# Optimization experiments

Measured on AMD Instinct MI355X. Metric: run time of the kernel, lower is better.

## Reference

```python
import jax, jax.numpy as jnp
import numpy as np

N = 768
SINGLE_DIM = 384
PAIR_DIM = 128
D = 16      # proj_dim per head
H = 12      # n_heads
P = 4       # n_query_points
PV = 8      # n_point_values


def _random_rotations(key, n):
    a = jax.random.normal(key, (n, 3, 3), dtype=jnp.float32)
    q, r = jnp.linalg.qr(a)
    d = jnp.sign(jnp.diagonal(r, axis1=-2, axis2=-1))
    q = q * d[:, None, :]
    det = jnp.linalg.det(q)
    return q * jnp.where(det < 0, -1.0, 1.0)[:, None, None]


def setup_inputs() -> dict:
    key = jax.random.key(0)
    ks = jax.random.split(key, 12)
    s = 0.02
    return {
        "single_rep": jax.random.normal(ks[0], (N, SINGLE_DIM), dtype=jnp.float32),
        "pair_rep": jax.random.normal(ks[1], (N, N, PAIR_DIM), dtype=jnp.float32),
        "rotations": _random_rotations(ks[2], N),
        "translations": jax.random.normal(ks[3], (N, 3), dtype=jnp.float32),
        "Wqkv": s * jax.random.normal(ks[4], (SINGLE_DIM, 3 * H * D), dtype=jnp.float32),
        "Wb": s * jax.random.normal(ks[5], (PAIR_DIM, H), dtype=jnp.float32),
        "Wqk_pts": s * jax.random.normal(ks[6], (SINGLE_DIM, 2 * H * P * 3), dtype=jnp.float32),
        "Wv_pts": s * jax.random.normal(ks[7], (SINGLE_DIM, H * PV * 3), dtype=jnp.float32),
        "gamma": 0.1 * jax.random.normal(ks[8], (H,), dtype=jnp.float32),
        "Wout": s * jax.random.normal(ks[9], (H * (PAIR_DIM + D + PV * 3 + PV), SINGLE_DIM), dtype=jnp.float32),
        "bout": jnp.zeros((SINGLE_DIM,), dtype=jnp.float32),
    }


def _apply_frames(rot, trans, pts):
    # pts: [N, P, H, 3] -> R @ pt + t per residue (dim 0)
    return jnp.einsum('nba,npha->nphb', rot, pts) + trans[:, None, None, :]


def _apply_frames_inv(rot, trans, pts):
    # R^T (pt - t)
    return jnp.einsum('nab,npha->nphb', rot, pts - trans[:, None, None, :])


def reference(single_rep, pair_rep, rotations, translations,
              Wqkv, Wb, Wqk_pts, Wv_pts, gamma, Wout, bout):
    n = single_rep.shape[0]
    sqrt_inv_dim = 1.0 / np.sqrt(D).astype(np.float32)
    w_C = np.sqrt(2.0 / (9.0 * P)).astype(np.float32)
    w_L = np.sqrt(1.0 / 3.0).astype(np.float32)

    qkv = single_rep @ Wqkv                       # [N, 3*H*D]
    q, k, v = jnp.split(qkv, 3, axis=-1)
    q = q.reshape(n, D, H)
    k = k.reshape(n, D, H)
    v = v.reshape(n, D, H)

    b = pair_rep @ Wb                             # [N, N, H]

    qk_pts = single_rep @ Wqk_pts
    q_pts, k_pts = jnp.split(qk_pts, 2, axis=-1)
    q_pts = jnp.moveaxis(q_pts.reshape(n, P, 3, H), -1, -2)   # [N, P, H, 3]
    k_pts = jnp.moveaxis(k_pts.reshape(n, P, 3, H), -1, -2)
    v_pts = jnp.moveaxis((single_rep @ Wv_pts).reshape(n, PV, 3, H), -1, -2)  # [N, PV, H, 3]

    qg = _apply_frames(rotations, translations, q_pts)  # [N, P, H, 3]
    kg = _apply_frames(rotations, translations, k_pts)

    # sum_{p,t} ||qg_i - kg_j||^2 via expansion (avoids [N,N,P,H,3])
    q_sq = jnp.sum(qg * qg, axis=(1, 3))                # [N, H]
    k_sq = jnp.sum(kg * kg, axis=(1, 3))                # [N, H]
    cross = jnp.einsum('ipht,jpht->ijh', qg, kg)        # [N, N, H]
    dist_logits = q_sq[:, None, :] + k_sq[None, :, :] - 2.0 * cross

    dp_logits = sqrt_inv_dim * jnp.einsum('idh,jdh->ijh', q, k) + b
    scale = gamma * (w_C / 2.0)                          # [H]
    a = jax.nn.softmax(w_L * (dp_logits - scale * dist_logits), axis=1)  # [N, N, H]

    out_pair = jnp.einsum('ijh,ijz->izh', a, pair_rep)   # [N, pair_dim, H]
    out_value = jnp.einsum('ijh,jdh->idh', a, v)          # [N, D, H]

    vg = _apply_frames(rotations, translations, v_pts)    # [N, PV, H, 3]
    op = jnp.einsum('ijh,jpht->ipht', a, vg)              # [N, PV, H, 3]
    out_points = _apply_frames_inv(rotations, translations, op)
    out_points_norm = jnp.linalg.norm(out_points, axis=-1)  # [N, PV, H]

    out = jnp.concatenate([
        out_pair.reshape(n, -1),
        out_value.reshape(n, -1),
        out_points.reshape(n, -1),
        out_points_norm.reshape(n, -1),
    ], axis=1)
    return out @ Wout + bout
```

## Files before the change

kernel.cpp:

```cpp
#include <hip/hip_runtime.h>
#include <math.h>

#define NN 768
#define SD 384
#define HH 12

#define W_L 0.57735026918962576f
#define W_C 0.23570226039551584f

__device__ __forceinline__ float dot32(const float* q, const float* k) {
  float s = 0.f;
  #pragma unroll
  for (int m = 0; m < 8; ++m) {
    float4 a = *(const float4*)(q + m*4);
    float4 b = *(const float4*)(k + m*4);
    s += a.x*b.x + a.y*b.y + a.z*b.z + a.w*b.w;
  }
  return s;
}

__global__ __launch_bounds__(256) void k1a_gemm(
    const float* __restrict__ single, const float* __restrict__ Wqkv,
    const float* __restrict__ Wqk, const float* __restrict__ Wvp,
    float* __restrict__ raw)
{
  __shared__ float Al[64][17];
  __shared__ float Bl[16][68];
  const int tid = threadIdx.x;
  const int bm = blockIdx.x / 18, bn = blockIdx.x % 18;
  const int tr = tid >> 4, tc = tid & 15;

  const int bcol = bn*64 + (tid & 15)*4;
  const float* Wsrc; int wstride;
  if (bcol < 576)      { Wsrc = Wqkv + bcol;        wstride = 576; }
  else if (bcol < 864) { Wsrc = Wqk  + (bcol-576);  wstride = 288; }
  else                 { Wsrc = Wvp  + (bcol-864);  wstride = 288; }
  const int brow = tid >> 4;
  const int ar = tid >> 2, ac = (tid & 3)*4;

  float4 acc0 = {0,0,0,0}, acc1 = {0,0,0,0}, acc2 = {0,0,0,0}, acc3 = {0,0,0,0};

  for (int kc = 0; kc < 24; ++kc) {
    __syncthreads();
    *(float4*)&Al[ar][ac] = *(const float4*)(single + (size_t)(bm*64+ar)*SD + kc*16 + ac);
    *(float4*)&Bl[brow][(tid&15)*4] = *(const float4*)(Wsrc + (size_t)(kc*16+brow)*wstride);
    __syncthreads();
    #pragma unroll
    for (int kk = 0; kk < 16; ++kk) {
      float a0 = Al[tr*4+0][kk], a1 = Al[tr*4+1][kk], a2 = Al[tr*4+2][kk], a3 = Al[tr*4+3][kk];
      float4 bv = *(float4*)&Bl[kk][tc*4];
      acc0.x += a0*bv.x; acc0.y += a0*bv.y; acc0.z += a0*bv.z; acc0.w += a0*bv.w;
      acc1.x += a1*bv.x; acc1.y += a1*bv.y; acc1.z += a1*bv.z; acc1.w += a1*bv.w;
      acc2.x += a2*bv.x; acc2.y += a2*bv.y; acc2.z += a2*bv.z; acc2.w += a2*bv.w;
      acc3.x += a3*bv.x; acc3.y += a3*bv.y; acc3.z += a3*bv.z; acc3.w += a3*bv.w;
    }
  }
  float* o = raw + (size_t)(bm*64 + tr*4)*1152 + bn*64 + tc*4;
  *(float4*)(o)            = acc0;
  *(float4*)(o + 1152)     = acc1;
  *(float4*)(o + 2*1152)   = acc2;
  *(float4*)(o + 3*1152)   = acc3;
}

__global__ __launch_bounds__(256) void k1b_pack(
    const float* __restrict__ raw_g, const float* __restrict__ rot,
    const float* __restrict__ trans, const float* __restrict__ gamma,
    float* __restrict__ Qt, float* __restrict__ Kt, float* __restrict__ vv)
{
  __shared__ float raw[4][1152];
  __shared__ float gbuf[4][16][HH][3];
  const int tid = threadIdx.x;
  const int i0 = blockIdx.x * 4;

  for (int s = tid; s < 4*288; s += 256) {
    int r = s / 288, q = s % 288;
    *(float4*)(&raw[r][q*4]) = *(const float4*)(raw_g + (size_t)(i0+r)*1152 + q*4);
  }
  __syncthreads();

  for (int s = tid; s < 4*576; s += 256) {
    int r = s / 576, cc = s % 576;
    int d = (cc % 192) / HH, h = cc % HH;
    int i = i0 + r;
    float val = raw[r][cc];
    if (cc < 192)       Qt[(size_t)i*384 + h*32 + d] = 0.25f*W_L*val;
    else if (cc < 384)  Kt[(size_t)i*384 + h*32 + d] = val;
    else                vv[(size_t)i*480 + h*40 + d] = val;
  }
  for (int s = tid; s < 768; s += 256) {
    int r = s / 192, rem = s % 192;
    int slot = rem / HH, h = rem % HH;
    int i = i0 + r;
    int base;
    if (slot < 4) base = 576 + slot*36;
    else if (slot < 8) base = 720 + (slot-4)*36;
    else base = 864 + (slot-8)*36;
    float x0 = raw[r][base + 0*12 + h];
    float x1 = raw[r][base + 1*12 + h];
    float x2 = raw[r][base + 2*12 + h];
    const float* R = rot + (size_t)i*9;
    const float* T = trans + (size_t)i*3;
    float g0 = R[0]*x0 + R[1]*x1 + R[2]*x2 + T[0];
    float g1 = R[3]*x0 + R[4]*x1 + R[5]*x2 + T[1];
    float g2 = R[6]*x0 + R[7]*x1 + R[8]*x2 + T[2];
    gbuf[r][slot][h][0]=g0; gbuf[r][slot][h][1]=g1; gbuf[r][slot][h][2]=g2;
    if (slot < 4) {
      float sc2 = 2.0f*W_L*(gamma[h]*W_C*0.5f);
      float* q = Qt + (size_t)i*384 + h*32 + 16 + slot*3;
      q[0]=sc2*g0; q[1]=sc2*g1; q[2]=sc2*g2;
    } else if (slot < 8) {
      float* k = Kt + (size_t)i*384 + h*32 + 16 + (slot-4)*3;
      k[0]=g0; k[1]=g1; k[2]=g2;
    } else {
      float* vp = vv + (size_t)i*480 + h*40 + 16 + (slot-8)*3;
      vp[0]=g0; vp[1]=g1; vp[2]=g2;
    }
  }
  __syncthreads();
  for (int s = tid; s < 96; s += 256) {
    int r = s / 24, rem = s % 24;
    int h = rem / 2, qk = rem % 2;
    int i = i0 + r;
    float sum = 0;
    int b0 = qk ? 4 : 0;
    for (int p = 0; p < 4; ++p)
      for (int t = 0; t < 3; ++t) { float g = gbuf[r][b0+p][h][t]; sum += g*g; }
    float sc = gamma[h]*W_C*0.5f;
    if (qk == 0) {
      float* q = Qt + (size_t)i*384 + h*32;
      q[28] = -W_L*sc; q[29] = -W_L*sc*sum; q[30] = 0.f; q[31] = 0.f;
    } else {
      float* k = Kt + (size_t)i*384 + h*32;
      k[28] = sum; k[29] = 1.f; k[30] = 0.f; k[31] = 0.f;
    }
  }
}

__global__ __launch_bounds__(256, 4) void k2f(
    const float* __restrict__ pair, const float* __restrict__ Wb,
    const float* __restrict__ Qt, const float* __restrict__ Kt,
    const float* __restrict__ vv, const float* __restrict__ rot,
    const float* __restrict__ trans, float* __restrict__ C2)
{
  __shared__ float Wl[1536];
  __shared__ float Qrow[384];
  __shared__ float Ta[32*68];
  __shared__ float Tb[32*68];
  __shared__ float part[4*12*33];
  __shared__ float plds[12*33];
  __shared__ float scl[12];
  __shared__ float smm[12], sms[12];
  __shared__ float oacc[480];

  const int tid = threadIdx.x;
  const int i = blockIdx.x;
  const int wave = tid >> 6;
  const int lane = tid & 63;
  const int jj = lane & 31;
  const int half = lane >> 5;

  for (int s = tid; s < 1536; s += 256) Wl[s] = Wb[s];
  for (int s = tid; s < 384; s += 256) Qrow[s] = Qt[(size_t)i*384 + s];
  if (tid < 12) { smm[tid] = -1e30f; sms[tid] = 0.f; }
  __syncthreads();

  const int zbase = wave*32 + half*16;
  const float* prow = pair + (size_t)i*NN*128;

  const int z4 = tid & 31, hgA = tid >> 5;
  float* TbaseA = ((z4 & 1) ? Tb : Ta) + ((z4 >> 1) * 4);
  const int lB = tid - 192;
  const int hB = (lB < 60 && lB >= 0) ? lB / 5 : 0;
  const int cgB = hB*40 + (((lB >= 0 ? lB : 0) % 5) * 8);

  float4 ra[4], rb[4];
  float accA[2][4] = {{0,0,0,0},{0,0,0,0}};
  float accB[8] = {0,0,0,0,0,0,0,0};

  {
    const float* src = prow + (size_t)jj*128 + zbase;
    ra[0] = *(const float4*)(src);
    ra[1] = *(const float4*)(src + 4);
    ra[2] = *(const float4*)(src + 8);
    ra[3] = *(const float4*)(src + 12);
  }

  auto iter = [&](int t, float4 (&cur)[4], float4 (&nxt)[4]) {
    const int j0 = t*32;
    if (t < 23) {
      const float* src = prow + (size_t)(j0 + 32 + jj)*128 + zbase;
      nxt[0] = *(const float4*)(src);
      nxt[1] = *(const float4*)(src + 4);
      nxt[2] = *(const float4*)(src + 8);
      nxt[3] = *(const float4*)(src + 12);
    }
    #pragma unroll
    for (int k = 0; k < 4; ++k) {
      const int z4w = wave*8 + half*4 + k;
      float* dst = ((z4w & 1) ? Tb : Ta) + jj*68 + (z4w >> 1)*4;
      *(float4*)dst = cur[k];
    }
    {
      float4 pb0 = {0,0,0,0}, pb1 = {0,0,0,0}, pb2 = {0,0,0,0};
      #pragma unroll
      for (int k = 0; k < 4; ++k) {
        #pragma unroll
        for (int e = 0; e < 4; ++e) {
          const float tv = (e==0) ? cur[k].x : (e==1) ? cur[k].y : (e==2) ? cur[k].z : cur[k].w;
          const float* w = &Wl[(zbase + k*4 + e)*12];
          float4 w0 = *(const float4*)(w);
          float4 w1 = *(const float4*)(w + 4);
          float4 w2 = *(const float4*)(w + 8);
          pb0.x += tv*w0.x; pb0.y += tv*w0.y; pb0.z += tv*w0.z; pb0.w += tv*w0.w;
          pb1.x += tv*w1.x; pb1.y += tv*w1.y; pb1.z += tv*w1.z; pb1.w += tv*w1.w;
          pb2.x += tv*w2.x; pb2.y += tv*w2.y; pb2.z += tv*w2.z; pb2.w += tv*w2.w;
        }
      }
      pb0.x += __shfl_xor(pb0.x, 32); pb0.y += __shfl_xor(pb0.y, 32);
      pb0.z += __shfl_xor(pb0.z, 32); pb0.w += __shfl_xor(pb0.w, 32);
      pb1.x += __shfl_xor(pb1.x, 32); pb1.y += __shfl_xor(pb1.y, 32);
      pb1.z += __shfl_xor(pb1.z, 32); pb1.w += __shfl_xor(pb1.w, 32);
      pb2.x += __shfl_xor(pb2.x, 32); pb2.y += __shfl_xor(pb2.y, 32);
      pb2.z += __shfl_xor(pb2.z, 32); pb2.w += __shfl_xor(pb2.w, 32);
      if (half == 0) {
        float* pp = part + (wave*12)*33 + jj;
        pp[0*33] = pb0.x; pp[1*33] = pb0.y; pp[2*33] = pb0.z; pp[3*33] = pb0.w;
        pp[4*33] = pb1.x; pp[5*33] = pb1.y; pp[6*33] = pb1.z; pp[7*33] = pb1.w;
        pp[8*33] = pb2.x; pp[9*33] = pb2.y; pp[10*33] = pb2.z; pp[11*33] = pb2.w;
      }
    }
    __syncthreads();
    {
      const int hg = tid >> 5, jc = tid & 31;
      const float* kr = Kt + (size_t)(j0 + jc)*384;
      {
        float d = dot32(&Qrow[hg*32], kr + hg*32);
        const float* pp = part + hg*33 + jc;
        float bs = pp[0] + pp[396] + pp[792] + pp[1188];
        plds[hg*33 + jc] = d + W_L*bs;
      }
      if (hg < 4) {
        const int h2 = hg + 8;
        float d = dot32(&Qrow[h2*32], kr + h2*32);
        const float* pp = part + h2*33 + jc;
        float bs = pp[0] + pp[396] + pp[792] + pp[1188];
        plds[h2*33 + jc] = d + W_L*bs;
      }
    }
    __syncthreads();
    if (tid < 48) {
      const int h = tid >> 2, q = tid & 3;
      float v0 = plds[h*33 + q*8 + 0], v1 = plds[h*33 + q*8 + 1];
      float v2 = plds[h*33 + q*8 + 2], v3 = plds[h*33 + q*8 + 3];
      float v4 = plds[h*33 + q*8 + 4], v5 = plds[h*33 + q*8 + 5];
      float v6 = plds[h*33 + q*8 + 6], v7 = plds[h*33 + q*8 + 7];
      float mt = fmaxf(fmaxf(fmaxf(v0,v1),fmaxf(v2,v3)), fmaxf(fmaxf(v4,v5),fmaxf(v6,v7)));
      mt = fmaxf(mt, __shfl_xor(mt, 1));
      mt = fmaxf(mt, __shfl_xor(mt, 2));
      float mo = smm[h];
      float mn = fmaxf(mo, mt);
      float sc = __expf(mo - mn);
      float p0 = __expf(v0-mn), p1 = __expf(v1-mn), p2 = __expf(v2-mn), p3 = __expf(v3-mn);
      float p4 = __expf(v4-mn), p5 = __expf(v5-mn), p6 = __expf(v6-mn), p7 = __expf(v7-mn);
      plds[h*33 + q*8 + 0] = p0; plds[h*33 + q*8 + 1] = p1;
      plds[h*33 + q*8 + 2] = p2; plds[h*33 + q*8 + 3] = p3;
      plds[h*33 + q*8 + 4] = p4; plds[h*33 + q*8 + 5] = p5;
      plds[h*33 + q*8 + 6] = p6; plds[h*33 + q*8 + 7] = p7;
      float ps = ((p0+p1)+(p2+p3)) + ((p4+p5)+(p6+p7));
      ps += __shfl_xor(ps, 1);
      ps += __shfl_xor(ps, 2);
      if (q == 0) { sms[h] = sms[h]*sc + ps; smm[h] = mn; scl[h] = sc; }
    }
    __syncthreads();
    if (tid < 192) {
      const int h0 = hgA*2;
      const float s0 = scl[h0], s1 = scl[h0+1];
      accA[0][0]*=s0; accA[0][1]*=s0; accA[0][2]*=s0; accA[0][3]*=s0;
      accA[1][0]*=s1; accA[1][1]*=s1; accA[1][2]*=s1; accA[1][3]*=s1;
      const float* p0p = &plds[h0*33];
      const float* p1p = &plds[(h0+1)*33];
      #pragma unroll 4
      for (int j2 = 0; j2 < 32; ++j2) {
        float4 tv = *(const float4*)(TbaseA + (size_t)j2*68);
        float p0 = p0p[j2], p1 = p1p[j2];
        accA[0][0] += p0*tv.x; accA[0][1] += p0*tv.y; accA[0][2] += p0*tv.z; accA[0][3] += p0*tv.w;
        accA[1][0] += p1*tv.x; accA[1][1] += p1*tv.y; accA[1][2] += p1*tv.z; accA[1][3] += p1*tv.w;
      }
    } else if (lB < 60) {
      const float sc = scl[hB];
      #pragma unroll
      for (int e = 0; e < 8; ++e) accB[e] *= sc;
      const float* pp = &plds[hB*33];
      const float* vp = vv + (size_t)j0*480 + cgB;
      #pragma unroll 4
      for (int j2 = 0; j2 < 32; ++j2) {
        float4 v0 = *(const float4*)(vp + (size_t)j2*480);
        float4 v1 = *(const float4*)(vp + (size_t)j2*480 + 4);
        float p = pp[j2];
        accB[0] += p*v0.x; accB[1] += p*v0.y; accB[2] += p*v0.z; accB[3] += p*v0.w;
        accB[4] += p*v1.x; accB[5] += p*v1.y; accB[6] += p*v1.z; accB[7] += p*v1.w;
      }
    }
    __syncthreads();
  };

  #pragma unroll 1
  for (int t2 = 0; t2 < 12; ++t2) {
    iter(2*t2,     ra, rb);
    iter(2*t2 + 1, rb, ra);
  }

  if (tid < 192) {
    const int h0 = hgA*2;
    const float i0v = 1.0f/sms[h0], i1v = 1.0f/sms[h0+1];
    float* o = C2 + (size_t)i*2112;
    #pragma unroll
    for (int e = 0; e < 4; ++e) {
      o[(z4*4+e)*12 + h0]   = accA[0][e]*i0v;
      o[(z4*4+e)*12 + h0+1] = accA[1][e]*i1v;
    }
  } else if (lB < 60) {
    const float inv = 1.0f/sms[hB];
    #pragma unroll
    for (int e = 0; e < 8; ++e) oacc[cgB+e] = accB[e]*inv;
  }
  __syncthreads();
  if (tid < 96) {
    const int pp = tid / 12, h = tid % 12;
    const float* R = rot + (size_t)i*9;
    const float* T = trans + (size_t)i*3;
    float x0 = oacc[h*40+16+pp*3+0] - T[0];
    float x1 = oacc[h*40+16+pp*3+1] - T[1];
    float x2 = oacc[h*40+16+pp*3+2] - T[2];
    float y0 = R[0]*x0 + R[3]*x1 + R[6]*x2;
    float y1 = R[1]*x0 + R[4]*x1 + R[7]*x2;
    float y2 = R[2]*x0 + R[5]*x1 + R[8]*x2;
    float* o = C2 + (size_t)i*2112;
    o[1728 + pp*36 + h*3 + 0] = y0;
    o[1728 + pp*36 + h*3 + 1] = y1;
    o[1728 + pp*36 + h*3 + 2] = y2;
    o[2016 + pp*12 + h] = sqrtf(y0*y0 + y1*y1 + y2*y2);
  } else if (tid < 192) {
    const int c = tid - 96;
    float* o = C2 + (size_t)i*2112 + 1536;
    o[c]      = oacc[(c%12)*40 + (c/12)];
    o[c+96]   = oacc[((c+96)%12)*40 + ((c+96)/12)];
  }
}

__global__ __launch_bounds__(256) void k5_out(
    const float* __restrict__ C2, const float* __restrict__ Wout,
    const float* __restrict__ bout, float* __restrict__ out)
{
  __shared__ float Al[32*68];
  __shared__ float Bl[64*36];
  const int tid = threadIdx.x;
  const int bm = blockIdx.x / 12, bn = blockIdx.x % 12;
  const int tr = tid / 16, tc = tid % 16;
  float acc00=0, acc01=0, acc10=0, acc11=0;
  for (int kc = 0; kc < 33; ++kc) {
    __syncthreads();
    for (int s = tid; s < 512; s += 256) {
      int row = s / 16, kq = s % 16;
      *(float4*)(&Al[row*68 + kq*4]) =
        *(const float4*)(C2 + (size_t)(bm*32+row)*2112 + kc*64 + kq*4);
    }
    for (int s = tid; s < 512; s += 256) {
      int kk = s / 8, cq = s % 8;
      *(float4*)(&Bl[kk*36 + cq*4]) =
        *(const float4*)(Wout + (size_t)(kc*64+kk)*384 + bn*32 + cq*4);
    }
    __syncthreads();
    for (int kk = 0; kk < 64; ++kk) {
      float a0 = Al[(tr*2)*68 + kk], a1 = Al[(tr*2+1)*68 + kk];
      float b0 = Bl[kk*36 + tc*2], b1 = Bl[kk*36 + tc*2 + 1];
      acc00 += a0*b0; acc01 += a0*b1;
      acc10 += a1*b0; acc11 += a1*b1;
    }
  }
  int r0 = bm*32 + tr*2, c0 = bn*32 + tc*2;
  out[(size_t)r0*384 + c0]       = acc00 + bout[c0];
  out[(size_t)r0*384 + c0+1]     = acc01 + bout[c0+1];
  out[(size_t)(r0+1)*384 + c0]   = acc10 + bout[c0];
  out[(size_t)(r0+1)*384 + c0+1] = acc11 + bout[c0+1];
}

extern "C" void kernel_launch(void* const* d_in, const int* in_sizes, int n_in,
                              void* d_out, int out_size, void* d_ws, size_t ws_size,
                              hipStream_t stream)
{
  const float* single = (const float*)d_in[0];
  const float* pair   = (const float*)d_in[1];
  const float* rot    = (const float*)d_in[2];
  const float* trans  = (const float*)d_in[3];
  const float* Wqkv   = (const float*)d_in[4];
  const float* Wb     = (const float*)d_in[5];
  const float* Wqk    = (const float*)d_in[6];
  const float* Wvp    = (const float*)d_in[7];
  const float* gamma  = (const float*)d_in[8];
  const float* Wout   = (const float*)d_in[9];
  const float* bout   = (const float*)d_in[10];

  float* ws  = (float*)d_ws;
  float* raw = ws;
  float* Qt  = raw + (size_t)768*1152;
  float* Kt  = Qt + (size_t)768*384;
  float* vv  = Kt + (size_t)768*384;
  float* C2  = vv + (size_t)768*480;
  float* out = (float*)d_out;

  k1a_gemm<<<dim3(216), dim3(256), 0, stream>>>(single, Wqkv, Wqk, Wvp, raw);
  k1b_pack<<<dim3(192), dim3(256), 0, stream>>>(raw, rot, trans, gamma, Qt, Kt, vv);
  k2f<<<dim3(768), dim3(256), 0, stream>>>(pair, Wb, Qt, Kt, vv, rot, trans, C2);
  k5_out<<<dim3(288), dim3(256), 0, stream>>>(C2, Wout, bout, out);
}
```

Baseline: 329.9 us.

## Move attention logits and pair aggregation onto bf16 MFMA with pipelined stages

The fused attention kernel now converts pair tiles to bf16 in LDS and computes the pair bias plus the q·k and point logits with bf16 MFMA instructions. The softmax-weighted pair aggregation also runs on MFMA. K is stored as bf16. The stages are software-pipelined so that logits for tile t overlap with aggregation of tile t-1, with double-buffered LDS. This aims to cut the scalar FMA cost of the dominant kernel, at the price of bf16 precision in the logits and aggregation, and a larger LDS footprint that may reduce occupancy.

```diff
diff --git a/kernel.cpp b/kernel.cpp
--- a/kernel.cpp
+++ b/kernel.cpp
@@ -8,15 +8,15 @@
 #define W_L 0.57735026918962576f
 #define W_C 0.23570226039551584f
 
-__device__ __forceinline__ float dot32(const float* q, const float* k) {
-  float s = 0.f;
-  #pragma unroll
-  for (int m = 0; m < 8; ++m) {
-    float4 a = *(const float4*)(q + m*4);
-    float4 b = *(const float4*)(k + m*4);
-    s += a.x*b.x + a.y*b.y + a.z*b.z + a.w*b.w;
-  }
-  return s;
+typedef __attribute__((ext_vector_type(8))) short short8;
+typedef __attribute__((ext_vector_type(4))) float floatx4;
+typedef unsigned short ushort_t;
+typedef unsigned int uint_t;
+
+static __device__ __forceinline__ ushort_t f2bf(float f) {
+  union { float f; uint_t u; } v; v.f = f;
+  uint_t r = (v.u + 0x7FFFu + ((v.u >> 16) & 1u)) >> 16;
+  return (ushort_t)r;
 }
 
 __global__ __launch_bounds__(256) void k1a_gemm(
@@ -65,7 +65,7 @@
 __global__ __launch_bounds__(256) void k1b_pack(
     const float* __restrict__ raw_g, const float* __restrict__ rot,
     const float* __restrict__ trans, const float* __restrict__ gamma,
-    float* __restrict__ Qt, float* __restrict__ Kt, float* __restrict__ vv)
+    float* __restrict__ Qt, ushort_t* __restrict__ Ktb, float* __restrict__ vv)
 {
   __shared__ float raw[4][1152];
   __shared__ float gbuf[4][16][HH][3];
@@ -84,7 +84,7 @@
     int i = i0 + r;
     float val = raw[r][cc];
     if (cc < 192)       Qt[(size_t)i*384 + h*32 + d] = 0.25f*W_L*val;
-    else if (cc < 384)  Kt[(size_t)i*384 + h*32 + d] = val;
+    else if (cc < 384)  Ktb[(size_t)i*384 + h*32 + d] = f2bf(val);
     else                vv[(size_t)i*480 + h*40 + d] = val;
   }
   for (int s = tid; s < 768; s += 256) {
@@ -109,8 +109,8 @@
       float* q = Qt + (size_t)i*384 + h*32 + 16 + slot*3;
       q[0]=sc2*g0; q[1]=sc2*g1; q[2]=sc2*g2;
     } else if (slot < 8) {
-      float* k = Kt + (size_t)i*384 + h*32 + 16 + (slot-4)*3;
-      k[0]=g0; k[1]=g1; k[2]=g2;
+      ushort_t* k = Ktb + (size_t)i*384 + h*32 + 16 + (slot-4)*3;
+      k[0]=f2bf(g0); k[1]=f2bf(g1); k[2]=f2bf(g2);
     } else {
       float* vp = vv + (size_t)i*480 + h*40 + 16 + (slot-8)*3;
       vp[0]=g0; vp[1]=g1; vp[2]=g2;
@@ -130,201 +130,188 @@
       float* q = Qt + (size_t)i*384 + h*32;
       q[28] = -W_L*sc; q[29] = -W_L*sc*sum; q[30] = 0.f; q[31] = 0.f;
     } else {
-      float* k = Kt + (size_t)i*384 + h*32;
-      k[28] = sum; k[29] = 1.f; k[30] = 0.f; k[31] = 0.f;
-    }
-  }
-}
-
-__global__ __launch_bounds__(256, 4) void k2f(
+      ushort_t* k = Ktb + (size_t)i*384 + h*32;
+      k[28] = f2bf(sum); k[29] = f2bf(1.f); k[30] = 0; k[31] = 0;
+    }
+  }
+}
+
+__global__ __launch_bounds__(256) void k2m(
     const float* __restrict__ pair, const float* __restrict__ Wb,
-    const float* __restrict__ Qt, const float* __restrict__ Kt,
+    const float* __restrict__ Qt, const ushort_t* __restrict__ Ktb,
     const float* __restrict__ vv, const float* __restrict__ rot,
     const float* __restrict__ trans, float* __restrict__ C2)
 {
-  __shared__ float Wl[1536];
+  __shared__ ushort_t Tjz[2][32*136];
+  __shared__ ushort_t Tzj[2][128*40];
+  __shared__ ushort_t WbT[16*136];
+  __shared__ ushort_t PT[16*40];
+  __shared__ float pl[12*33];
+  __shared__ float lL[32*17];
   __shared__ float Qrow[384];
-  __shared__ float Ta[32*68];
-  __shared__ float Tb[32*68];
-  __shared__ float part[4*12*33];
-  __shared__ float plds[12*33];
-  __shared__ float scl[12];
-  __shared__ float smm[12], sms[12];
+  __shared__ float smm[16], sms[16], scl[16];
   __shared__ float oacc[480];
 
   const int tid = threadIdx.x;
   const int i = blockIdx.x;
-  const int wave = tid >> 6;
   const int lane = tid & 63;
-  const int jj = lane & 31;
-  const int half = lane >> 5;
-
-  for (int s = tid; s < 1536; s += 256) Wl[s] = Wb[s];
+  const int wv = tid >> 6;
+  const int sj = tid & 31, szq = tid >> 5;
+  const int co = lane & 15, gg = lane >> 4;
+
+  for (int s = tid; s < 1536; s += 256) {
+    int z = s / 12, h = s % 12;
+    WbT[h*136 + z] = f2bf(W_L * Wb[s]);
+  }
+  for (int s = tid; s < 4*136; s += 256) WbT[(12 + s/136)*136 + (s%136)] = 0;
+  for (int s = tid; s < 16*40; s += 256) PT[s] = 0;
   for (int s = tid; s < 384; s += 256) Qrow[s] = Qt[(size_t)i*384 + s];
-  if (tid < 12) { smm[tid] = -1e30f; sms[tid] = 0.f; }
+  if (tid < 16) { smm[tid] = -1e30f; sms[tid] = 0.f; scl[tid] = 0.f; }
   __syncthreads();
 
-  const int zbase = wave*32 + half*16;
-  const float* prow = pair + (size_t)i*NN*128;
-
-  const int z4 = tid & 31, hgA = tid >> 5;
-  float* TbaseA = ((z4 & 1) ? Tb : Ta) + ((z4 >> 1) * 4);
-  const int lB = tid - 192;
-  const int hB = (lB < 60 && lB >= 0) ? lB / 5 : 0;
-  const int cgB = hB*40 + (((lB >= 0 ? lB : 0) % 5) * 8);
-
-  float4 ra[4], rb[4];
-  float accA[2][4] = {{0,0,0,0},{0,0,0,0}};
-  float accB[8] = {0,0,0,0,0,0,0,0};
-
+  short8 myQ; short8 z8;
+  #pragma unroll
+  for (int s = 0; s < 8; ++s) z8[s] = 0;
+  #pragma unroll
+  for (int s = 0; s < 8; ++s)
+    myQ[s] = (co < 12) ? (short)f2bf(Qrow[co*32 + gg*8 + s]) : (short)0;
+
+  const float* psrc = pair + (size_t)i*NN*128;
+
+  float4 cur[4], nxt[4];
   {
-    const float* src = prow + (size_t)jj*128 + zbase;
-    ra[0] = *(const float4*)(src);
-    ra[1] = *(const float4*)(src + 4);
-    ra[2] = *(const float4*)(src + 8);
-    ra[3] = *(const float4*)(src + 12);
-  }
-
-  auto iter = [&](int t, float4 (&cur)[4], float4 (&nxt)[4]) {
-    const int j0 = t*32;
-    if (t < 23) {
-      const float* src = prow + (size_t)(j0 + 32 + jj)*128 + zbase;
-      nxt[0] = *(const float4*)(src);
-      nxt[1] = *(const float4*)(src + 4);
-      nxt[2] = *(const float4*)(src + 8);
-      nxt[3] = *(const float4*)(src + 12);
-    }
-    #pragma unroll
-    for (int k = 0; k < 4; ++k) {
-      const int z4w = wave*8 + half*4 + k;
-      float* dst = ((z4w & 1) ? Tb : Ta) + jj*68 + (z4w >> 1)*4;
-      *(float4*)dst = cur[k];
-    }
-    {
-      float4 pb0 = {0,0,0,0}, pb1 = {0,0,0,0}, pb2 = {0,0,0,0};
-      #pragma unroll
-      for (int k = 0; k < 4; ++k) {
+    const float* s0 = psrc + (size_t)sj*128 + szq*16;
+    cur[0] = *(const float4*)(s0);     cur[1] = *(const float4*)(s0+4);
+    cur[2] = *(const float4*)(s0+8);   cur[3] = *(const float4*)(s0+12);
+  }
+
+  floatx4 accP[8];
+  #pragma unroll
+  for (int n = 0; n < 8; ++n) { accP[n][0]=0.f; accP[n][1]=0.f; accP[n][2]=0.f; accP[n][3]=0.f; }
+  float accB[4] = {0,0,0,0};
+  const int tid2 = tid - 128;
+  const int c0 = (tid2 >= 0 && tid2 < 120) ? tid2*4 : 0;
+  const int hB = c0 / 40;
+
+  for (int t = 0; t <= 24; ++t) {
+    const int buf = t & 1;
+    if (t < 24) {
+      if (t < 23) {
+        const float* sn = psrc + (size_t)(t+1)*32*128 + (size_t)sj*128 + szq*16;
+        nxt[0] = *(const float4*)(sn);     nxt[1] = *(const float4*)(sn+4);
+        nxt[2] = *(const float4*)(sn+8);   nxt[3] = *(const float4*)(sn+12);
+      }
+      const float* cf = (const float*)cur;
+      ushort_t bb[16];
+      #pragma unroll
+      for (int e = 0; e < 16; ++e) bb[e] = f2bf(cf[e]);
+      short8 w0, w1;
+      #pragma unroll
+      for (int e = 0; e < 8; ++e) { w0[e] = (short)bb[e]; w1[e] = (short)bb[8+e]; }
+      *(short8*)&Tjz[buf][sj*136 + szq*16]     = w0;
+      *(short8*)&Tjz[buf][sj*136 + szq*16 + 8] = w1;
+      #pragma unroll
+      for (int e = 0; e < 16; ++e) Tzj[buf][(szq*16 + e)*40 + sj] = bb[e];
+    }
+    __syncthreads();
+
+    if (t < 24 && wv == 1) {
+      #pragma unroll
+      for (int Mt = 0; Mt < 2; ++Mt) {
+        floatx4 D; D[0]=0.f; D[1]=0.f; D[2]=0.f; D[3]=0.f;
+        const int jr = Mt*16 + co;
         #pragma unroll
-        for (int e = 0; e < 4; ++e) {
-          const float tv = (e==0) ? cur[k].x : (e==1) ? cur[k].y : (e==2) ? cur[k].z : cur[k].w;
-          const float* w = &Wl[(zbase + k*4 + e)*12];
-          float4 w0 = *(const float4*)(w);
-          float4 w1 = *(const float4*)(w + 4);
-          float4 w2 = *(const float4*)(w + 8);
-          pb0.x += tv*w0.x; pb0.y += tv*w0.y; pb0.z += tv*w0.z; pb0.w += tv*w0.w;
-          pb1.x += tv*w1.x; pb1.y += tv*w1.y; pb1.z += tv*w1.z; pb1.w += tv*w1.w;
-          pb2.x += tv*w2.x; pb2.y += tv*w2.y; pb2.z += tv*w2.z; pb2.w += tv*w2.w;
+        for (int kt = 0; kt < 4; ++kt) {
+          short8 a = *(const short8*)&Tjz[buf][jr*136 + kt*32 + gg*8];
+          short8 b = *(const short8*)&WbT[co*136 + kt*32 + gg*8];
+          D = __builtin_amdgcn_mfma_f32_16x16x32_bf16(a, b, D, 0, 0, 0);
+        }
+        const ushort_t* kr = Ktb + (size_t)(t*32 + jr)*384;
+        #pragma unroll
+        for (int kt = 0; kt < 12; ++kt) {
+          short8 a = *(const short8*)(kr + kt*32 + gg*8);
+          short8 b = (co == kt) ? myQ : z8;
+          D = __builtin_amdgcn_mfma_f32_16x16x32_bf16(a, b, D, 0, 0, 0);
+        }
+        #pragma unroll
+        for (int r = 0; r < 4; ++r) lL[(Mt*16 + gg*4 + r)*17 + co] = D[r];
+      }
+    }
+    if (t > 0) {
+      const int pbuf = (t-1) & 1;
+      if (wv == 0) {
+        float s4[4];
+        #pragma unroll
+        for (int r = 0; r < 4; ++r) s4[r] = scl[gg*4 + r];
+        short8 aP = *(const short8*)&PT[co*40 + gg*8];
+        #pragma unroll
+        for (int Nt = 0; Nt < 8; ++Nt) {
+          floatx4 aa = accP[Nt];
+          aa[0]*=s4[0]; aa[1]*=s4[1]; aa[2]*=s4[2]; aa[3]*=s4[3];
+          short8 bT = *(const short8*)&Tzj[pbuf][(Nt*16 + co)*40 + gg*8];
+          accP[Nt] = __builtin_amdgcn_mfma_f32_16x16x32_bf16(aP, bT, aa, 0, 0, 0);
+        }
+      } else if (wv >= 2 && tid2 < 120) {
+        float sc = scl[hB];
+        accB[0]*=sc; accB[1]*=sc; accB[2]*=sc; accB[3]*=sc;
+        const int j0 = (t-1)*32;
+        const float* vp = vv + (size_t)j0*480 + c0;
+        #pragma unroll 4
+        for (int jj = 0; jj < 32; ++jj) {
+          float p = pl[hB*33 + jj];
+          float4 v = *(const float4*)(vp + (size_t)jj*480);
+          accB[0] += p*v.x; accB[1] += p*v.y; accB[2] += p*v.z; accB[3] += p*v.w;
         }
       }
-      pb0.x += __shfl_xor(pb0.x, 32); pb0.y += __shfl_xor(pb0.y, 32);
-      pb0.z += __shfl_xor(pb0.z, 32); pb0.w += __shfl_xor(pb0.w, 32);
-      pb1.x += __shfl_xor(pb1.x, 32); pb1.y += __shfl_xor(pb1.y, 32);
-      pb1.z += __shfl_xor(pb1.z, 32); pb1.w += __shfl_xor(pb1.w, 32);
-      pb2.x += __shfl_xor(pb2.x, 32); pb2.y += __shfl_xor(pb2.y, 32);
-      pb2.z += __shfl_xor(pb2.z, 32); pb2.w += __shfl_xor(pb2.w, 32);
-      if (half == 0) {
-        float* pp = part + (wave*12)*33 + jj;
-        pp[0*33] = pb0.x; pp[1*33] = pb0.y; pp[2*33] = pb0.z; pp[3*33] = pb0.w;
-        pp[4*33] = pb1.x; pp[5*33] = pb1.y; pp[6*33] = pb1.z; pp[7*33] = pb1.w;
-        pp[8*33] = pb2.x; pp[9*33] = pb2.y; pp[10*33] = pb2.z; pp[11*33] = pb2.w;
-      }
-    }
-    __syncthreads();
-    {
-      const int hg = tid >> 5, jc = tid & 31;
-      const float* kr = Kt + (size_t)(j0 + jc)*384;
-      {
-        float d = dot32(&Qrow[hg*32], kr + hg*32);
-        const float* pp = part + hg*33 + jc;
-        float bs = pp[0] + pp[396] + pp[792] + pp[1188];
-        plds[hg*33 + jc] = d + W_L*bs;
-      }
-      if (hg < 4) {
-        const int h2 = hg + 8;
-        float d = dot32(&Qrow[h2*32], kr + h2*32);
-        const float* pp = part + h2*33 + jc;
-        float bs = pp[0] + pp[396] + pp[792] + pp[1188];
-        plds[h2*33 + jc] = d + W_L*bs;
-      }
-    }
-    __syncthreads();
-    if (tid < 48) {
-      const int h = tid >> 2, q = tid & 3;
-      float v0 = plds[h*33 + q*8 + 0], v1 = plds[h*33 + q*8 + 1];
-      float v2 = plds[h*33 + q*8 + 2], v3 = plds[h*33 + q*8 + 3];
-      float v4 = plds[h*33 + q*8 + 4], v5 = plds[h*33 + q*8 + 5];
-      float v6 = plds[h*33 + q*8 + 6], v7 = plds[h*33 + q*8 + 7];
-      float mt = fmaxf(fmaxf(fmaxf(v0,v1),fmaxf(v2,v3)), fmaxf(fmaxf(v4,v5),fmaxf(v6,v7)));
+    }
+    __syncthreads();
+
+    if (t < 24 && wv == 0 && lane < 48) {
+      const int h = lane >> 2, q = lane & 3;
+      float v[8];
+      #pragma unroll
+      for (int e = 0; e < 8; ++e) v[e] = lL[(q*8 + e)*17 + h];
+      float mt = fmaxf(fmaxf(fmaxf(v[0],v[1]),fmaxf(v[2],v[3])),
+                       fmaxf(fmaxf(v[4],v[5]),fmaxf(v[6],v[7])));
       mt = fmaxf(mt, __shfl_xor(mt, 1));
       mt = fmaxf(mt, __shfl_xor(mt, 2));
       float mo = smm[h];
       float mn = fmaxf(mo, mt);
       float sc = __expf(mo - mn);
-      float p0 = __expf(v0-mn), p1 = __expf(v1-mn), p2 = __expf(v2-mn), p3 = __expf(v3-mn);
-      float p4 = __expf(v4-mn), p5 = __expf(v5-mn), p6 = __expf(v6-mn), p7 = __expf(v7-mn);
-      plds[h*33 + q*8 + 0] = p0; plds[h*33 + q*8 + 1] = p1;
-      plds[h*33 + q*8 + 2] = p2; plds[h*33 + q*8 + 3] = p3;
-      plds[h*33 + q*8 + 4] = p4; plds[h*33 + q*8 + 5] = p5;
-      plds[h*33 + q*8 + 6] = p6; plds[h*33 + q*8 + 7] = p7;
-      float ps = ((p0+p1)+(p2+p3)) + ((p4+p5)+(p6+p7));
+      float ps = 0.f;
+      #pragma unroll
+      for (int e = 0; e < 8; ++e) {
+        float p = __expf(v[e] - mn);
+        pl[h*33 + q*8 + e] = p;
+        PT[h*40 + q*8 + e] = f2bf(p);
+        ps += p;
+      }
       ps += __shfl_xor(ps, 1);
       ps += __shfl_xor(ps, 2);
       if (q == 0) { sms[h] = sms[h]*sc + ps; smm[h] = mn; scl[h] = sc; }
     }
     __syncthreads();
-    if (tid < 192) {
-      const int h0 = hgA*2;
-      const float s0 = scl[h0], s1 = scl[h0+1];
-      accA[0][0]*=s0; accA[0][1]*=s0; accA[0][2]*=s0; accA[0][3]*=s0;
-      accA[1][0]*=s1; accA[1][1]*=s1; accA[1][2]*=s1; accA[1][3]*=s1;
-      const float* p0p = &plds[h0*33];
-      const float* p1p = &plds[(h0+1)*33];
-      #pragma unroll 4
-      for (int j2 = 0; j2 < 32; ++j2) {
-        float4 tv = *(const float4*)(TbaseA + (size_t)j2*68);
-        float p0 = p0p[j2], p1 = p1p[j2];
-        accA[0][0] += p0*tv.x; accA[0][1] += p0*tv.y; accA[0][2] += p0*tv.z; accA[0][3] += p0*tv.w;
-        accA[1][0] += p1*tv.x; accA[1][1] += p1*tv.y; accA[1][2] += p1*tv.z; accA[1][3] += p1*tv.w;
-      }
-    } else if (lB < 60) {
-      const float sc = scl[hB];
-      #pragma unroll
-      for (int e = 0; e < 8; ++e) accB[e] *= sc;
-      const float* pp = &plds[hB*33];
-      const float* vp = vv + (size_t)j0*480 + cgB;
-      #pragma unroll 4
-      for (int j2 = 0; j2 < 32; ++j2) {
-        float4 v0 = *(const float4*)(vp + (size_t)j2*480);
-        float4 v1 = *(const float4*)(vp + (size_t)j2*480 + 4);
-        float p = pp[j2];
-        accB[0] += p*v0.x; accB[1] += p*v0.y; accB[2] += p*v0.z; accB[3] += p*v0.w;
-        accB[4] += p*v1.x; accB[5] += p*v1.y; accB[6] += p*v1.z; accB[7] += p*v1.w;
-      }
-    }
-    __syncthreads();
-  };
-
-  #pragma unroll 1
-  for (int t2 = 0; t2 < 12; ++t2) {
-    iter(2*t2,     ra, rb);
-    iter(2*t2 + 1, rb, ra);
-  }
-
-  if (tid < 192) {
-    const int h0 = hgA*2;
-    const float i0v = 1.0f/sms[h0], i1v = 1.0f/sms[h0+1];
+
+    if (t < 23) { cur[0]=nxt[0]; cur[1]=nxt[1]; cur[2]=nxt[2]; cur[3]=nxt[3]; }
+  }
+
+  if (wv == 0) {
     float* o = C2 + (size_t)i*2112;
     #pragma unroll
-    for (int e = 0; e < 4; ++e) {
-      o[(z4*4+e)*12 + h0]   = accA[0][e]*i0v;
-      o[(z4*4+e)*12 + h0+1] = accA[1][e]*i1v;
-    }
-  } else if (lB < 60) {
-    const float inv = 1.0f/sms[hB];
+    for (int Nt = 0; Nt < 8; ++Nt) {
+      #pragma unroll
+      for (int r = 0; r < 4; ++r) {
+        int h = gg*4 + r;
+        if (h < 12) o[(Nt*16 + co)*12 + h] = accP[Nt][r] / sms[h];
+      }
+    }
+  } else if (wv >= 2 && tid2 < 120) {
+    float inv = 1.0f / sms[hB];
     #pragma unroll
-    for (int e = 0; e < 8; ++e) oacc[cgB+e] = accB[e]*inv;
+    for (int e = 0; e < 4; ++e) oacc[c0 + e] = accB[e]*inv;
   }
   __syncthreads();
+
   if (tid < 96) {
     const int pp = tid / 12, h = tid % 12;
     const float* R = rot + (size_t)i*9;
@@ -401,16 +388,16 @@
   const float* Wout   = (const float*)d_in[9];
   const float* bout   = (const float*)d_in[10];
 
-  float* ws  = (float*)d_ws;
-  float* raw = ws;
-  float* Qt  = raw + (size_t)768*1152;
-  float* Kt  = Qt + (size_t)768*384;
-  float* vv  = Kt + (size_t)768*384;
-  float* C2  = vv + (size_t)768*480;
-  float* out = (float*)d_out;
+  float* ws   = (float*)d_ws;
+  float* raw  = ws;
+  float* Qt   = raw + (size_t)768*1152;
+  float* vvp  = Qt + (size_t)768*384;
+  float* C2   = vvp + (size_t)768*480;
+  ushort_t* Ktb = (ushort_t*)(C2 + (size_t)768*2112);
+  float* out  = (float*)d_out;
 
   k1a_gemm<<<dim3(216), dim3(256), 0, stream>>>(single, Wqkv, Wqk, Wvp, raw);
-  k1b_pack<<<dim3(192), dim3(256), 0, stream>>>(raw, rot, trans, gamma, Qt, Kt, vv);
-  k2f<<<dim3(768), dim3(256), 0, stream>>>(pair, Wb, Qt, Kt, vv, rot, trans, C2);
+  k1b_pack<<<dim3(192), dim3(256), 0, stream>>>(raw, rot, trans, gamma, Qt, Ktb, vvp);
+  k2m<<<dim3(768), dim3(256), 0, stream>>>(pair, Wb, Qt, Ktb, vvp, rot, trans, C2);
   k5_out<<<dim3(288), dim3(256), 0, stream>>>(C2, Wout, bout, out);
 }
```

New measurement: 352.5 us. +6.9%, slower.
